# Kernel tuning notes

Measured on AMD Instinct MI355X. Metric: run time of the kernel, lower is better.

The kernel has to match this reference:

```python
import jax, jax.numpy as jnp
import numpy as np

# Module hyperparameters (from init_kwargs)
KH, KW = 3, 3        # kernel_size
SH, SW = 1, 1        # stride
PH, PW = 1, 1        # padding
NUM_ITER = 3         # num_iterations


def squash(t, axis=-1):
    # scale = |t|^2 / (1 + |t|^2); out = scale * t / |t|
    sq = jnp.sum(t * t, axis=axis, keepdims=True)
    return (sq / (1.0 + sq)) * t / jnp.sqrt(sq)


def setup_inputs() -> dict:
    key = jax.random.key(0)
    k1, k2 = jax.random.split(key)
    x = jax.random.normal(k1, (4, 32, 56, 56), dtype=jnp.float32)
    # weight: (P_out, P_in, K, L_in, L_out) = (64//16, 32//8, 3*3, 8, 16)
    # (the original stores an extra size-1 dim at position 2; squeezed here)
    weight = jax.random.normal(k2, (4, 4, 9, 8, 16), dtype=jnp.float32)
    return {"x": x, "weight": weight}


def reference(x, weight):
    N, C_in, H, W = x.shape
    P_out, P_in, K, L_in, L_out = weight.shape
    H_out = (H + 2 * PH - KH) // SH + 1
    W_out = (W + 2 * PW - KW) // SW + 1

    # im2col: (N, C_in, H_out, W_out, K)
    xp = jnp.pad(x, ((0, 0), (0, 0), (PH, PH), (PW, PW)))
    patches = jnp.stack(
        [xp[:, :, dj:dj + SH * H_out:SH, dk:dk + SW * W_out:SW]
         for dj in range(KH) for dk in range(KW)],
        axis=-1,
    )
    # split channels into capsule planes: (N, P_in, L_in, H_out, W_out, K)
    patches = patches.reshape(N, P_in, L_in, H_out, W_out, K)

    # priors[n,o,p,h,w,k,:] = window[n,p,h,w,k,:] @ weight[o,p,k,:,:]
    priors = jnp.einsum('nplhwk,opkld->nophwkd', patches, weight)

    # dynamic routing. logits broadcast over the L_out dim in the original
    # (delta_logits has a keepdim size-1 last axis), so track them as (...,K,1).
    logits = jnp.zeros(priors.shape[:-1] + (1,), priors.dtype)
    outputs = None
    for i in range(NUM_ITER):
        probs = jax.nn.softmax(logits, axis=-2)          # softmax over K
        s = jnp.sum(probs * priors, axis=-2, keepdims=True)  # (...,1,L_out)
        outputs = squash(s, axis=-1)
        if i != NUM_ITER - 1:
            logits = logits + jnp.sum(priors * outputs, axis=-1, keepdims=True)

    # sum routed outputs over input capsule planes (the .add accumulation)
    out = jnp.sum(outputs[..., 0, :], axis=2)            # (N, P_out, H_out, W_out, L_out)
    out = jnp.transpose(out, (0, 1, 4, 2, 3)).reshape(N, P_out * L_out, H_out, W_out)
    return out
```

## Files before the change

### kernel.cpp

```cpp
#include <hip/hip_runtime.h>


#define HW 56
#define HW2 3136
#define WSTRIDE 1168
#define XSTR 33
#define XN (60 * XSTR)

__device__ __forceinline__ float quad_add1(float x) {
    int y = __builtin_amdgcn_update_dpp(0, __float_as_int(x), 0xB1, 0xF, 0xF, true);
    return x + __int_as_float(y);
}
__device__ __forceinline__ float quad_add2(float x) {
    int y = __builtin_amdgcn_update_dpp(0, __float_as_int(x), 0x4E, 0xF, 0xF, true);
    return x + __int_as_float(y);
}
__device__ __forceinline__ float quad_reduce(float x) {
    return quad_add2(quad_add1(x));
}

__global__ void caps_routing_kernel(
    const float* __restrict__ x, const float* __restrict__ wgt,
    float* __restrict__ out)
{
    __shared__ float lds_w[4 * WSTRIDE];
    __shared__ float lds_x[XN];

    const int tid = threadIdx.x;
    const int bx  = blockIdx.x;
    const int n = bx >> 2, o = bx & 3;

    const int by = blockIdx.y;
    const int hb = by / 7;
    const int wb = by - hb * 7;
    const int h0 = hb * 4;
    const int w0 = wb * 8;

    {
        const float4* wsrc = (const float4*)(wgt + o * 4608);
        for (int i = tid; i < 1152; i += 256) {
            const int pp  = i / 288;
            const int rem = i - pp * 288;
            *(float4*)&lds_w[pp * WSTRIDE + rem * 4] = wsrc[i];
        }
    }
    {
        const float* xn = x + n * 32 * HW2;
        for (int idx = tid; idx < 1920; idx += 256) {
            const int ch  = idx / 60;
            const int rem = idx - ch * 60;
            const int r   = rem / 10;
            const int c   = rem - r * 10;
            const int gr  = h0 - 1 + r;
            const int gc  = w0 - 1 + c;
            float v = 0.f;
            if ((unsigned)gr < (unsigned)HW && (unsigned)gc < (unsigned)HW)
                v = xn[ch * HW2 + gr * HW + gc];
            lds_x[rem * XSTR + ch] = v;
        }
    }
    __syncthreads();

    const int dq = tid & 3;
    const int wl = (tid >> 2) & 3;
    const int p  = (tid >> 4) & 3;
    const int wi = tid >> 6;
    const int hh = wi >> 1, ww = wi & 1;

    float M[9][4][2];
    #pragma unroll
    for (int k = 0; k < 9; ++k)
        #pragma unroll
        for (int j = 0; j < 4; ++j) { M[k][j][0] = 0.f; M[k][j][1] = 0.f; }

    const float* xb  = &lds_x[((hh * 2) * 10 + ww * 4 + wl) * XSTR + p * 8];
    const float* wbp = &lds_w[p * WSTRIDE + dq * 4];

    #pragma clang loop unroll(disable)
    for (int l = 0; l < 8; ++l) {
        const float* xl  = xb + l;
        const float* wlp = wbp + l * 16;
        float xv[4][3];
        #pragma unroll
        for (int rr = 0; rr < 4; ++rr)
            #pragma unroll
            for (int c = 0; c < 3; ++c)
                xv[rr][c] = xl[(rr * 10 + c) * XSTR];
        #pragma unroll
        for (int rr = 0; rr < 3; ++rr) {
            #pragma unroll
            for (int kc = 0; kc < 3; ++kc) {
                const int k = rr * 3 + kc;
                const float4 wa = *(const float4*)(wlp + k * 128);
                const float xs0 = xv[rr][kc];
                const float xs1 = xv[rr + 1][kc];
                M[k][0][0] += xs0 * wa.x; M[k][1][0] += xs0 * wa.y;
                M[k][2][0] += xs0 * wa.z; M[k][3][0] += xs0 * wa.w;
                M[k][0][1] += xs1 * wa.x; M[k][1][1] += xs1 * wa.y;
                M[k][2][1] += xs1 * wa.z; M[k][3][1] += xs1 * wa.w;
            }
        }
    }

    #pragma unroll
    for (int ti = 0; ti < 2; ++ti) {
        float v[4], b[9];
        {
            float s[4];
            #pragma unroll
            for (int j = 0; j < 4; ++j) {
                float a = M[0][j][ti];
                #pragma unroll
                for (int k = 1; k < 9; ++k) a += M[k][j][ti];
                s[j] = a * (1.f / 9.f);
            }
            float sq = s[0]*s[0] + s[1]*s[1] + s[2]*s[2] + s[3]*s[3];
            sq = quad_reduce(sq);
            const float scale = sq * __builtin_amdgcn_rsqf(sq) * __builtin_amdgcn_rcpf(1.f + sq);
            #pragma unroll
            for (int j = 0; j < 4; ++j) v[j] = s[j] * scale;
            #pragma unroll
            for (int k = 0; k < 9; ++k) {
                float u = M[k][0][ti]*v[0] + M[k][1][ti]*v[1]
                        + M[k][2][ti]*v[2] + M[k][3][ti]*v[3];
                b[k] = quad_reduce(u);
            }
        }

        #pragma unroll
        for (int it = 1; it < 3; ++it) {
            float mx = b[0];
            #pragma unroll
            for (int k = 1; k < 9; ++k) mx = fmaxf(mx, b[k]);
            float e[9]; float se = 0.f;
            #pragma unroll
            for (int k = 0; k < 9; ++k) { e[k] = __expf(b[k] - mx); se += e[k]; }
            const float inv = __builtin_amdgcn_rcpf(se);
            float s[4];
            #pragma unroll
            for (int j = 0; j < 4; ++j) {
                float a = 0.f;
                #pragma unroll
                for (int k = 0; k < 9; ++k) a += e[k] * M[k][j][ti];
                s[j] = a * inv;
            }
            float sq = s[0]*s[0] + s[1]*s[1] + s[2]*s[2] + s[3]*s[3];
            sq = quad_reduce(sq);
            const float scale = sq * __builtin_amdgcn_rsqf(sq) * __builtin_amdgcn_rcpf(1.f + sq);
            #pragma unroll
            for (int j = 0; j < 4; ++j) v[j] = s[j] * scale;
            if (it == 1) {
                #pragma unroll
                for (int k = 0; k < 9; ++k) {
                    float u = M[k][0][ti]*v[0] + M[k][1][ti]*v[1]
                            + M[k][2][ti]*v[2] + M[k][3][ti]*v[3];
                    b[k] += quad_reduce(u);
                }
            }
        }

        #pragma unroll
        for (int j = 0; j < 4; ++j) {
            v[j] += __shfl_xor(v[j], 16, 64);
            v[j] += __shfl_xor(v[j], 32, 64);
        }
        if (p == 0) {
            float* op = out + ((n * 64 + o * 16 + dq * 4) * HW + (h0 + hh * 2 + ti)) * HW
                      + w0 + ww * 4 + wl;
            #pragma unroll
            for (int j = 0; j < 4; ++j) op[j * HW2] = v[j];
        }
    }
}

extern "C" void kernel_launch(void* const* d_in, const int* in_sizes, int n_in,
                              void* d_out, int out_size, void* d_ws, size_t ws_size,
                              hipStream_t stream) {
    const float* x   = (const float*)d_in[0];
    const float* wgt = (const float*)d_in[1];
    float* out = (float*)d_out;

    caps_routing_kernel<<<dim3(16, 98), dim3(256), 0, stream>>>(x, wgt, out);
}
```

Before: 79.07 us.

## Halve spatial tile per block to one output row per thread

Reduces each block's tile from 4x8 to 2x8 outputs so every thread computes a single output position instead of two, halving the M accumulator registers and doubling the grid. The aim is higher occupancy and more parallelism for the routing math. In exchange, each block reloads the full weight slice into LDS and a relatively larger x halo, so global/LDS load traffic per output increases.

```diff
diff --git a/kernel.cpp b/kernel.cpp
--- a/kernel.cpp
+++ b/kernel.cpp
@@ -5,7 +5,7 @@
 #define HW2 3136
 #define WSTRIDE 1168
 #define XSTR 33
-#define XN (60 * XSTR)
+#define XN (40 * XSTR)
 
 __device__ __forceinline__ float quad_add1(float x) {
     int y = __builtin_amdgcn_update_dpp(0, __float_as_int(x), 0xB1, 0xF, 0xF, true);
@@ -33,7 +33,7 @@
     const int by = blockIdx.y;
     const int hb = by / 7;
     const int wb = by - hb * 7;
-    const int h0 = hb * 4;
+    const int h0 = hb * 2;
     const int w0 = wb * 8;
 
     {
@@ -46,9 +46,9 @@
     }
     {
         const float* xn = x + n * 32 * HW2;
-        for (int idx = tid; idx < 1920; idx += 256) {
-            const int ch  = idx / 60;
-            const int rem = idx - ch * 60;
+        for (int idx = tid; idx < 1280; idx += 256) {
+            const int ch  = idx / 40;
+            const int rem = idx - ch * 40;
             const int r   = rem / 10;
             const int c   = rem - r * 10;
             const int gr  = h0 - 1 + r;
@@ -67,22 +67,22 @@
     const int wi = tid >> 6;
     const int hh = wi >> 1, ww = wi & 1;
 
-    float M[9][4][2];
+    float M[9][4];
     #pragma unroll
     for (int k = 0; k < 9; ++k)
         #pragma unroll
-        for (int j = 0; j < 4; ++j) { M[k][j][0] = 0.f; M[k][j][1] = 0.f; }
+        for (int j = 0; j < 4; ++j) M[k][j] = 0.f;
 
-    const float* xb  = &lds_x[((hh * 2) * 10 + ww * 4 + wl) * XSTR + p * 8];
+    const float* xb  = &lds_x[(hh * 10 + ww * 4 + wl) * XSTR + p * 8];
     const float* wbp = &lds_w[p * WSTRIDE + dq * 4];
 
     #pragma clang loop unroll(disable)
     for (int l = 0; l < 8; ++l) {
         const float* xl  = xb + l;
         const float* wlp = wbp + l * 16;
-        float xv[4][3];
+        float xv[3][3];
         #pragma unroll
-        for (int rr = 0; rr < 4; ++rr)
+        for (int rr = 0; rr < 3; ++rr)
             #pragma unroll
             for (int c = 0; c < 3; ++c)
                 xv[rr][c] = xl[(rr * 10 + c) * XSTR];
@@ -92,84 +92,76 @@
             for (int kc = 0; kc < 3; ++kc) {
                 const int k = rr * 3 + kc;
                 const float4 wa = *(const float4*)(wlp + k * 128);
-                const float xs0 = xv[rr][kc];
-                const float xs1 = xv[rr + 1][kc];
-                M[k][0][0] += xs0 * wa.x; M[k][1][0] += xs0 * wa.y;
-                M[k][2][0] += xs0 * wa.z; M[k][3][0] += xs0 * wa.w;
-                M[k][0][1] += xs1 * wa.x; M[k][1][1] += xs1 * wa.y;
-                M[k][2][1] += xs1 * wa.z; M[k][3][1] += xs1 * wa.w;
+                const float xs = xv[rr][kc];
+                M[k][0] += xs * wa.x; M[k][1] += xs * wa.y;
+                M[k][2] += xs * wa.z; M[k][3] += xs * wa.w;
+            }
+        }
+    }
+
+    float v[4], b[9];
+    {
+        float s[4];
+        #pragma unroll
+        for (int j = 0; j < 4; ++j) {
+            float a = M[0][j];
+            #pragma unroll
+            for (int k = 1; k < 9; ++k) a += M[k][j];
+            s[j] = a * (1.f / 9.f);
+        }
+        float sq = s[0]*s[0] + s[1]*s[1] + s[2]*s[2] + s[3]*s[3];
+        sq = quad_reduce(sq);
+        const float scale = sq * __builtin_amdgcn_rsqf(sq) * __builtin_amdgcn_rcpf(1.f + sq);
+        #pragma unroll
+        for (int j = 0; j < 4; ++j) v[j] = s[j] * scale;
+        #pragma unroll
+        for (int k = 0; k < 9; ++k) {
+            float u = M[k][0]*v[0] + M[k][1]*v[1] + M[k][2]*v[2] + M[k][3]*v[3];
+            b[k] = quad_reduce(u);
+        }
+    }
+
+    #pragma unroll
+    for (int it = 1; it < 3; ++it) {
+        float mx = b[0];
+        #pragma unroll
+        for (int k = 1; k < 9; ++k) mx = fmaxf(mx, b[k]);
+        float e[9]; float se = 0.f;
+        #pragma unroll
+        for (int k = 0; k < 9; ++k) { e[k] = __expf(b[k] - mx); se += e[k]; }
+        const float inv = __builtin_amdgcn_rcpf(se);
+        float s[4];
+        #pragma unroll
+        for (int j = 0; j < 4; ++j) {
+            float a = 0.f;
+            #pragma unroll
+            for (int k = 0; k < 9; ++k) a += e[k] * M[k][j];
+            s[j] = a * inv;
+        }
+        float sq = s[0]*s[0] + s[1]*s[1] + s[2]*s[2] + s[3]*s[3];
+        sq = quad_reduce(sq);
+        const float scale = sq * __builtin_amdgcn_rsqf(sq) * __builtin_amdgcn_rcpf(1.f + sq);
+        #pragma unroll
+        for (int j = 0; j < 4; ++j) v[j] = s[j] * scale;
+        if (it == 1) {
+            #pragma unroll
+            for (int k = 0; k < 9; ++k) {
+                float u = M[k][0]*v[0] + M[k][1]*v[1] + M[k][2]*v[2] + M[k][3]*v[3];
+                b[k] += quad_reduce(u);
             }
         }
     }
 
     #pragma unroll
-    for (int ti = 0; ti < 2; ++ti) {
-        float v[4], b[9];
-        {
-            float s[4];
-            #pragma unroll
-            for (int j = 0; j < 4; ++j) {
-                float a = M[0][j][ti];
-                #pragma unroll
-                for (int k = 1; k < 9; ++k) a += M[k][j][ti];
-                s[j] = a * (1.f / 9.f);
-            }
-            float sq = s[0]*s[0] + s[1]*s[1] + s[2]*s[2] + s[3]*s[3];
-            sq = quad_reduce(sq);
-            const float scale = sq * __builtin_amdgcn_rsqf(sq) * __builtin_amdgcn_rcpf(1.f + sq);
-            #pragma unroll
-            for (int j = 0; j < 4; ++j) v[j] = s[j] * scale;
-            #pragma unroll
-            for (int k = 0; k < 9; ++k) {
-                float u = M[k][0][ti]*v[0] + M[k][1][ti]*v[1]
-                        + M[k][2][ti]*v[2] + M[k][3][ti]*v[3];
-                b[k] = quad_reduce(u);
-            }
-        }
-
+    for (int j = 0; j < 4; ++j) {
+        v[j] += __shfl_xor(v[j], 16, 64);
+        v[j] += __shfl_xor(v[j], 32, 64);
+    }
+    if (p == 0) {
+        float* op = out + ((n * 64 + o * 16 + dq * 4) * HW + (h0 + hh)) * HW
+                  + w0 + ww * 4 + wl;
         #pragma unroll
-        for (int it = 1; it < 3; ++it) {
-            float mx = b[0];
-            #pragma unroll
-            for (int k = 1; k < 9; ++k) mx = fmaxf(mx, b[k]);
-            float e[9]; float se = 0.f;
-            #pragma unroll
-            for (int k = 0; k < 9; ++k) { e[k] = __expf(b[k] - mx); se += e[k]; }
-            const float inv = __builtin_amdgcn_rcpf(se);
-            float s[4];
-            #pragma unroll
-            for (int j = 0; j < 4; ++j) {
-                float a = 0.f;
-                #pragma unroll
-                for (int k = 0; k < 9; ++k) a += e[k] * M[k][j][ti];
-                s[j] = a * inv;
-            }
-            float sq = s[0]*s[0] + s[1]*s[1] + s[2]*s[2] + s[3]*s[3];
-            sq = quad_reduce(sq);
-            const float scale = sq * __builtin_amdgcn_rsqf(sq) * __builtin_amdgcn_rcpf(1.f + sq);
-            #pragma unroll
-            for (int j = 0; j < 4; ++j) v[j] = s[j] * scale;
-            if (it == 1) {
-                #pragma unroll
-                for (int k = 0; k < 9; ++k) {
-                    float u = M[k][0][ti]*v[0] + M[k][1][ti]*v[1]
-                            + M[k][2][ti]*v[2] + M[k][3][ti]*v[3];
-                    b[k] += quad_reduce(u);
-                }
-            }
-        }
-
-        #pragma unroll
-        for (int j = 0; j < 4; ++j) {
-            v[j] += __shfl_xor(v[j], 16, 64);
-            v[j] += __shfl_xor(v[j], 32, 64);
-        }
-        if (p == 0) {
-            float* op = out + ((n * 64 + o * 16 + dq * 4) * HW + (h0 + hh * 2 + ti)) * HW
-                      + w0 + ww * 4 + wl;
-            #pragma unroll
-            for (int j = 0; j < 4; ++j) op[j * HW2] = v[j];
-        }
+        for (int j = 0; j < 4; ++j) op[j * HW2] = v[j];
     }
 }
 
@@ -180,5 +172,5 @@
     const float* wgt = (const float*)d_in[1];
     float* out = (float*)d_out;
 
-    caps_routing_kernel<<<dim3(16, 98), dim3(256), 0, stream>>>(x, wgt, out);
+    caps_routing_kernel<<<dim3(16, 196), dim3(256), 0, stream>>>(x, wgt, out);
 }
```

Measured after the change: 81.81 us. 3.5% more time.
